# Performance work log

Hardware: AMD Instinct MI355X
Metric: run time of the kernel (lower is better)

## Reference

```python
import jax, jax.numpy as jnp
import numpy as np

D_INNER, D_STATE, DT_RANK, D_CONV, NBLK = 256, 8, 8, 4, 3

def _conv2d(x, w, b=None):
    y = jax.lax.conv_general_dilated(x, w, (1, 1), 'SAME', dimension_numbers=('NCHW', 'OIHW', 'NCHW'))
    return y if b is None else y + b[None, :, None, None]

def _ln(x, g, b, eps=1e-5):
    m = x.mean(-1, keepdims=True)
    v = x.var(-1, keepdims=True)
    return (x - m) / jnp.sqrt(v + eps) * g + b

def _bn(x, g, b, m, v, eps=1e-5):
    return (x - m[None, :, None, None]) / jnp.sqrt(v[None, :, None, None] + eps) * g[None, :, None, None] + b[None, :, None, None]

def _up2(x):
    return jnp.repeat(jnp.repeat(x, 2, axis=2), 2, axis=3)

def _silu(x):
    return x * jax.nn.sigmoid(x)

def _selective_scan(u, dt, A, Bm, Cm):
    # u, dt: (B,L,D); A: (D,N); Bm, Cm: (B,L,N)
    dA = jnp.exp(dt[..., None] * A)              # (B,L,D,N)
    dBu = (dt * u)[..., None] * Bm[:, :, None, :]
    h0 = jnp.zeros((u.shape[0], u.shape[2], A.shape[1]), u.dtype)
    def step(h, inp):
        dA_t, dBu_t, C_t = inp
        h = dA_t * h + dBu_t
        return h, jnp.einsum('bdn,bn->bd', h, C_t)
    _, ys = jax.lax.scan(step, h0, (jnp.moveaxis(dA, 1, 0), jnp.moveaxis(dBu, 1, 0), jnp.moveaxis(Cm, 1, 0)))
    return jnp.moveaxis(ys, 0, 1)                # (B,L,D)

def _mamba(x, in_w, conv_w, conv_b, xproj_w, dt_w, dt_b, Alog, Dp, out_w):
    xz = jnp.einsum('bld,ed->ble', x, in_w)      # (B,L,2*D_INNER)
    xm, z = jnp.split(xz, 2, axis=-1)
    xc = jnp.moveaxis(xm, 1, 2)                  # (B,D,L)
    xc = jax.lax.conv_general_dilated(xc, conv_w[:, None, :], (1,), [(D_CONV - 1, 0)], dimension_numbers=('NCH', 'OIH', 'NCH'), feature_group_count=D_INNER)
    xm = _silu(jnp.moveaxis(xc + conv_b[None, :, None], 2, 1))
    xdbl = jnp.einsum('bld,ed->ble', xm, xproj_w)
    dt, Bm, Cm = jnp.split(xdbl, [DT_RANK, DT_RANK + D_STATE], axis=-1)
    dt = jax.nn.softplus(jnp.einsum('blr,dr->bld', dt, dt_w) + dt_b)
    A = -jnp.exp(Alog)
    y = _selective_scan(xm, dt, A, Bm, Cm) + xm * Dp
    y = y * _silu(z)
    return jnp.einsum('bld,od->blo', y, out_w)

def _cce(inp, ref, w1, w2):
    a = _conv2d(inp, w1)
    r = _conv2d(ref, w2)
    gate = jax.nn.sigmoid(a.max(axis=(2, 3), keepdims=True) + a.mean(axis=(2, 3), keepdims=True))
    return r * gate


def setup_inputs() -> dict:
    key = jax.random.key(0)
    ks = jax.random.split(key, 24)
    s = 0.05
    inp = {}
    inp['fused'] = jax.random.normal(ks[0], (16, 1024, 128), jnp.float32)
    inp['orig_x'] = jax.random.uniform(ks[1], (16, 32, 128, 128), jnp.float32)
    inp['orig_y'] = jax.random.uniform(ks[2], (16, 32, 128, 128), jnp.float32)
    inp['m_ln_g'] = jnp.ones((NBLK, 128), jnp.float32)
    inp['m_ln_b'] = jnp.zeros((NBLK, 128), jnp.float32)
    inp['m_in_w'] = jax.random.normal(ks[3], (NBLK, 2 * D_INNER, 128), jnp.float32) * s
    inp['m_conv_w'] = jax.random.normal(ks[4], (NBLK, D_INNER, D_CONV), jnp.float32) * s
    inp['m_conv_b'] = jnp.zeros((NBLK, D_INNER), jnp.float32)
    inp['m_xproj_w'] = jax.random.normal(ks[5], (NBLK, DT_RANK + 2 * D_STATE, D_INNER), jnp.float32) * s
    inp['m_dt_w'] = jax.random.normal(ks[6], (NBLK, D_INNER, DT_RANK), jnp.float32) * s
    inp['m_dt_b'] = jax.random.normal(ks[7], (NBLK, D_INNER), jnp.float32) * 0.1
    inp['m_Alog'] = jnp.log(jnp.broadcast_to(jnp.arange(1, D_STATE + 1, dtype=jnp.float32), (NBLK, D_INNER, D_STATE)))
    inp['m_D'] = jnp.ones((NBLK, D_INNER), jnp.float32)
    inp['m_out_w'] = jax.random.normal(ks[8], (NBLK, 128, D_INNER), jnp.float32) * s
    inp['lnf_g'] = jnp.ones((128,), jnp.float32)
    inp['lnf_b'] = jnp.zeros((128,), jnp.float32)
    inp['c1_w'] = jax.random.normal(ks[9], (64, 128, 3, 3), jnp.float32) * s
    inp['c1_b'] = jnp.zeros((64,), jnp.float32)
    inp['bn1_g'] = jnp.ones((64,), jnp.float32)
    inp['bn1_b'] = jnp.zeros((64,), jnp.float32)
    inp['bn1_m'] = jnp.zeros((64,), jnp.float32)
    inp['bn1_v'] = jnp.ones((64,), jnp.float32)
    inp['c2_w'] = jax.random.normal(ks[10], (32, 64, 3, 3), jnp.float32) * s
    inp['c2_b'] = jnp.zeros((32,), jnp.float32)
    inp['bn2_g'] = jnp.ones((32,), jnp.float32)
    inp['bn2_b'] = jnp.zeros((32,), jnp.float32)
    inp['bn2_m'] = jnp.zeros((32,), jnp.float32)
    inp['bn2_v'] = jnp.ones((32,), jnp.float32)
    inp['cce_w1'] = jax.random.normal(ks[11], (32, 32, 1, 1), jnp.float32) * s
    inp['cce_w2'] = jax.random.normal(ks[12], (32, 32, 1, 1), jnp.float32) * s
    inp['c3_w'] = jax.random.normal(ks[13], (1, 32, 3, 3), jnp.float32) * s
    inp['c3_b'] = jnp.zeros((1,), jnp.float32)
    return inp


def reference(fused, orig_x, orig_y, m_ln_g, m_ln_b, m_in_w, m_conv_w, m_conv_b, m_xproj_w, m_dt_w, m_dt_b, m_Alog, m_D, m_out_w, lnf_g, lnf_b, c1_w, c1_b, bn1_g, bn1_b, bn1_m, bn1_v, c2_w, c2_b, bn2_g, bn2_b, bn2_m, bn2_v, cce_w1, cce_w2, c3_w, c3_b):
    # 3 pre-LN Mamba blocks with residual connections
    for i in range(NBLK):
        skip = fused
        h = _ln(fused, m_ln_g[i], m_ln_b[i])
        fused = _mamba(h, m_in_w[i], m_conv_w[i], m_conv_b[i], m_xproj_w[i], m_dt_w[i], m_dt_b[i], m_Alog[i], m_D[i], m_out_w[i]) + skip
    fused = _ln(fused, lnf_g, lnf_b)
    B = fused.shape[0]
    fused = jnp.transpose(fused.reshape(B, 32, 32, 128), (0, 3, 1, 2))  # b c h w
    fused = _up2(fused)
    fused = jax.nn.relu(_bn(_conv2d(fused, c1_w, c1_b), bn1_g, bn1_b, bn1_m, bn1_v))
    fused = _up2(fused)
    fused = _bn(jax.nn.relu(_conv2d(fused, c2_w, c2_b)), bn2_g, bn2_b, bn2_m, bn2_v)
    fused = fused + _cce(orig_x, orig_y, cce_w1, cce_w2)
    fused = fused + _cce(orig_y, orig_x, cce_w1, cce_w2)
    return jax.nn.sigmoid(_conv2d(fused, c3_w, c3_b))
```

## Files before the change

kernel.cpp:

```cpp
#include <hip/hip_runtime.h>
#include <hip/hip_bf16.h>

#define BB   16
#define LL   1024
#define DM   128
#define DIN  256
#define NST  8
#define NROWS (BB*LL)
#define NCH  32
#define TCH  32
#define PSZ  1048576

static __device__ __forceinline__ float sigmoidf_(float x){ return 1.f/(1.f+expf(-x)); }
static __device__ __forceinline__ float siluf_(float x){ return x/(1.f+expf(-x)); }
static __device__ __forceinline__ unsigned short f2bf(float f){
    union { float f; unsigned u; } v; v.f = f;
    unsigned r = v.u + 0x7fff + ((v.u >> 16) & 1);
    return (unsigned short)(r >> 16);
}

typedef __attribute__((ext_vector_type(8))) short short8;
typedef __attribute__((ext_vector_type(4))) float floatx4;

__global__ __launch_bounds__(64) void ln_kernel(const float* __restrict__ X,
        const float* __restrict__ g, const float* __restrict__ b,
        float* __restrict__ Y, int transpose)
{
    int row = blockIdx.x;
    int t = threadIdx.x;
    float x0 = X[(long)row*DM + t];
    float x1 = X[(long)row*DM + 64 + t];
    float s = x0 + x1, ss = x0*x0 + x1*x1;
    #pragma unroll
    for (int off = 32; off; off >>= 1) { s += __shfl_down(s, off); ss += __shfl_down(ss, off); }
    s = __shfl(s, 0); ss = __shfl(ss, 0);
    float mean = s * (1.f/128.f);
    float var  = ss * (1.f/128.f) - mean*mean;
    float inv  = rsqrtf(var + 1e-5f);
    float y0 = (x0-mean)*inv*g[t]    + b[t];
    float y1 = (x1-mean)*inv*g[64+t] + b[64+t];
    if (!transpose) {
        Y[(long)row*DM + t] = y0;
        Y[(long)row*DM + 64 + t] = y1;
    } else {
        int bb = row >> 10, l = row & 1023;
        Y[((long)(bb*DM) + t)*LL + l] = y0;
        Y[((long)(bb*DM) + 64 + t)*LL + l] = y1;
    }
}

__global__ __launch_bounds__(64) void ln_bf16_kernel(const float* __restrict__ X,
        const float* __restrict__ g, const float* __restrict__ b,
        unsigned short* __restrict__ Y)
{
    int row = blockIdx.x;
    int t = threadIdx.x;
    float x0 = X[(long)row*DM + t];
    float x1 = X[(long)row*DM + 64 + t];
    float s = x0 + x1, ss = x0*x0 + x1*x1;
    #pragma unroll
    for (int off = 32; off; off >>= 1) { s += __shfl_down(s, off); ss += __shfl_down(ss, off); }
    s = __shfl(s, 0); ss = __shfl(ss, 0);
    float mean = s * (1.f/128.f);
    float var  = ss * (1.f/128.f) - mean*mean;
    float inv  = rsqrtf(var + 1e-5f);
    Y[(long)row*DM + t]      = f2bf((x0-mean)*inv*g[t]    + b[t]);
    Y[(long)row*DM + 64 + t] = f2bf((x1-mean)*inv*g[64+t] + b[64+t]);
}

__global__ void wcvt(const float* __restrict__ Win, const float* __restrict__ Wout,
                     unsigned short* __restrict__ Wb)
{
    int t = blockIdx.x*256 + threadIdx.x;
    if (t < 196608) Wb[t] = f2bf(Win[t]);
    else if (t < 294912) Wb[t] = f2bf(Wout[t - 196608]);
}

template<int K, int MT>
__global__ __launch_bounds__(256) void gemm_bf16(const unsigned short* __restrict__ A,
        const unsigned short* __restrict__ Wb, const float* __restrict__ S,
        float* __restrict__ C, int N)
{
    constexpr int NMT = MT/64;
    __shared__ unsigned short Als[MT][40];
    __shared__ unsigned short Bls[128][40];
    const int tid = threadIdx.x;
    const int m0 = blockIdx.x * MT;
    const int n0 = blockIdx.y * 128;
    const int lane = tid & 63, wv = tid >> 6;
    const int fr = lane & 15, quad = lane >> 4;
    floatx4 acc[NMT][8];
    #pragma unroll
    for (int mt = 0; mt < NMT; mt++)
        #pragma unroll
        for (int nt = 0; nt < 8; nt++) acc[mt][nt] = (floatx4){0.f,0.f,0.f,0.f};
    for (int kc = 0; kc < K; kc += 32) {
        __syncthreads();
        #pragma unroll
        for (int u = tid; u < MT*4; u += 256) {
            int row = u >> 2, seg = u & 3;
            *(uint4*)&Als[row][seg*8] = *(const uint4*)&A[(long)(m0+row)*K + kc + seg*8];
        }
        #pragma unroll
        for (int u = tid; u < 512; u += 256) {
            int row = u >> 2, seg = u & 3;
            *(uint4*)&Bls[row][seg*8] = *(const uint4*)&Wb[(long)(n0+row)*K + kc + seg*8];
        }
        __syncthreads();
        short8 af[NMT];
        #pragma unroll
        for (int mt = 0; mt < NMT; mt++)
            af[mt] = *(const short8*)&Als[wv*(16*NMT) + mt*16 + fr][quad*8];
        #pragma unroll
        for (int nt = 0; nt < 8; nt++) {
            short8 bfv = *(const short8*)&Bls[nt*16 + fr][quad*8];
            #pragma unroll
            for (int mt = 0; mt < NMT; mt++)
                acc[mt][nt] = __builtin_amdgcn_mfma_f32_16x16x32_bf16(af[mt], bfv, acc[mt][nt], 0, 0, 0);
        }
    }
    const int rq = quad * 4;
    #pragma unroll
    for (int mt = 0; mt < NMT; mt++)
        #pragma unroll
        for (int nt = 0; nt < 8; nt++)
            #pragma unroll
            for (int r = 0; r < 4; r++) {
                long m = m0 + wv*(16*NMT) + mt*16 + rq + r;
                long n = n0 + nt*16 + fr;
                float v = acc[mt][nt][r];
                if (S) v += S[m*N + n];
                C[m*N + n] = v;
            }
}

__global__ __launch_bounds__(256) void dwconv_xproj(const float* __restrict__ xz,
        const float* __restrict__ cw, const float* __restrict__ cb,
        const float* __restrict__ xproj_w, const float* __restrict__ dt_w,
        const float* __restrict__ dt_b, float* __restrict__ xc,
        float* __restrict__ dt_out, float* __restrict__ BC)
{
    __shared__ float xs[DIN];
    __shared__ float xdbl[24];
    int bl = blockIdx.x;
    int d  = threadIdx.x;
    int l  = bl & 1023;
    float w0 = cw[d*4+0], w1 = cw[d*4+1], w2 = cw[d*4+2], w3 = cw[d*4+3];
    const float* base = xz + (long)bl*512 + d;
    float acc = cb[d] + w3 * base[0];
    if (l >= 1) acc += w2 * base[-512];
    if (l >= 2) acc += w1 * base[-1024];
    if (l >= 3) acc += w0 * base[-1536];
    float u = siluf_(acc);
    xs[d] = u;
    xc[(long)bl*DIN + d] = u;
    __syncthreads();
    int t = d;
    if (t < 192) {
        int e = t >> 3, j = t & 7;
        float p = 0.f;
        for (int k = j; k < DIN; k += 8) p += xs[k] * xproj_w[e*DIN + k];
        p += __shfl_down(p, 4, 8);
        p += __shfl_down(p, 2, 8);
        p += __shfl_down(p, 1, 8);
        if (j == 0) xdbl[e] = p;
    }
    __syncthreads();
    float v = dt_b[d];
    #pragma unroll
    for (int r = 0; r < 8; r++) v += xdbl[r] * dt_w[d*8 + r];
    v = (v > 20.f) ? v : log1pf(expf(v));
    dt_out[(long)bl*DIN + d] = v;
    if (t < 16) BC[(long)bl*16 + t] = xdbl[8 + t];
}

__global__ __launch_bounds__(256) void scan_part(const float* __restrict__ dt,
        const float* __restrict__ xc, const float* __restrict__ BC,
        const float* __restrict__ Alog, float* __restrict__ PS)
{
    int b = blockIdx.x, c = blockIdx.y;
    int d = threadIdx.x;
    float a[NST], P[NST], S[NST];
    #pragma unroll
    for (int n = 0; n < NST; n++) { a[n] = -expf(Alog[d*NST + n]); P[n] = 1.f; S[n] = 0.f; }
    int t0 = c*TCH;
    const float* dtp = dt + ((long)b*LL + t0)*DIN + d;
    const float* up  = xc + ((long)b*LL + t0)*DIN + d;
    const float* bc  = BC + ((long)b*LL + t0)*16;
    for (int t = 0; t < TCH; t++) {
        float dtv = dtp[(long)t*DIN];
        float u   = up[(long)t*DIN];
        const float4* bc4 = (const float4*)(bc + t*16);
        float4 B0 = bc4[0], B1 = bc4[1];
        float Bv[NST] = {B0.x,B0.y,B0.z,B0.w,B1.x,B1.y,B1.z,B1.w};
        float dtu = dtv * u;
        #pragma unroll
        for (int n = 0; n < NST; n++) {
            float dA = __expf(dtv * a[n]);
            S[n] = dA * S[n] + dtu * Bv[n];
            P[n] *= dA;
        }
    }
    long o = (((long)b*NCH + c)*DIN + d)*8;
    #pragma unroll
    for (int n = 0; n < NST; n++) { PS[o + n] = P[n]; PS[PSZ + o + n] = S[n]; }
}

__global__ __launch_bounds__(256) void scan_mid(const float* __restrict__ PS,
        float* __restrict__ Hinit)
{
    int b = blockIdx.x;
    int n = blockIdx.y;
    int d = threadIdx.x;
    float h = 0.f;
    for (int c = 0; c < NCH; c++) {
        long o = (((long)b*NCH + c)*DIN + d)*8 + n;
        Hinit[o] = h;
        h = PS[o] * h + PS[PSZ + o];
    }
}

__global__ __launch_bounds__(256) void scan_fin(const float* __restrict__ dt,
        const float* __restrict__ xc, const float* __restrict__ BC,
        const float* __restrict__ xz, const float* __restrict__ Alog,
        const float* __restrict__ Dp, const float* __restrict__ Hinit,
        unsigned short* __restrict__ yg)
{
    int b = blockIdx.x, c = blockIdx.y;
    int d = threadIdx.x;
    float a[NST], h[NST];
    long o = (((long)b*NCH + c)*DIN + d)*8;
    #pragma unroll
    for (int n = 0; n < NST; n++) { a[n] = -expf(Alog[d*NST + n]); h[n] = Hinit[o + n]; }
    float Dpd = Dp[d];
    int t0 = c*TCH;
    const float* dtp = dt + ((long)b*LL + t0)*DIN + d;
    const float* up  = xc + ((long)b*LL + t0)*DIN + d;
    const float* bc  = BC + ((long)b*LL + t0)*16;
    const float* zp  = xz + ((long)b*LL + t0)*512 + 256 + d;
    unsigned short* yo = yg + ((long)b*LL + t0)*DIN + d;
    for (int t = 0; t < TCH; t++) {
        float dtv = dtp[(long)t*DIN];
        float u   = up[(long)t*DIN];
        const float4* bc4 = (const float4*)(bc + t*16);
        float4 B0 = bc4[0], B1 = bc4[1], C0 = bc4[2], C1 = bc4[3];
        float Bv[NST] = {B0.x,B0.y,B0.z,B0.w,B1.x,B1.y,B1.z,B1.w};
        float Cv[NST] = {C0.x,C0.y,C0.z,C0.w,C1.x,C1.y,C1.z,C1.w};
        float dtu = dtv * u;
        float y = 0.f;
        #pragma unroll
        for (int n = 0; n < NST; n++) {
            float dA = __expf(dtv * a[n]);
            h[n] = dA * h[n] + dtu * Bv[n];
            y += h[n] * Cv[n];
        }
        y += u * Dpd;
        float z = zp[(long)t*512];
        yo[(long)t*DIN] = f2bf(y * siluf_(z));
    }
}

__global__ void prep_weff(const float* __restrict__ Wr, float* __restrict__ We, int total)
{
    int t = blockIdx.x*256 + threadIdx.x;
    if (t >= total) return;
    float w[3][3];
    #pragma unroll
    for (int a = 0; a < 3; a++)
        #pragma unroll
        for (int c = 0; c < 3; c++) w[a][c] = Wr[(long)t*9 + a*3 + c];
    float cw[2][3][2];
    #pragma unroll
    for (int ky = 0; ky < 3; ky++) {
        cw[0][ky][0] = w[ky][0];           cw[0][ky][1] = w[ky][1] + w[ky][2];
        cw[1][ky][0] = w[ky][0] + w[ky][1]; cw[1][ky][1] = w[ky][2];
    }
    float* o = We + (long)t*16;
    #pragma unroll
    for (int px = 0; px < 2; px++) {
        o[0*8+px*4+0] = cw[px][0][0];               o[0*8+px*4+1] = cw[px][0][1];
        o[0*8+px*4+2] = cw[px][1][0]+cw[px][2][0];  o[0*8+px*4+3] = cw[px][1][1]+cw[px][2][1];
        o[1*8+px*4+0] = cw[px][0][0]+cw[px][1][0];  o[1*8+px*4+1] = cw[px][0][1]+cw[px][1][1];
        o[1*8+px*4+2] = cw[px][2][0];               o[1*8+px*4+3] = cw[px][2][1];
    }
}

template<int CIN, int INW, int ICB>
__global__ __launch_bounds__(256) void conv_up2_phase(const float* __restrict__ X,
        const float* __restrict__ We, const float* __restrict__ bias,
        const float* __restrict__ bng, const float* __restrict__ bnb,
        const float* __restrict__ bnm, const float* __restrict__ bnv,
        float* __restrict__ Y, int relu_first, int COUT)
{
    constexpr int OUTW = 2*INW;
    constexpr int NXT  = OUTW/64;
    __shared__ float  src[ICB][6][34];
    __shared__ float4 wf[ICB][16][4];
    const int ys = blockIdx.x / NXT, xt = blockIdx.x % NXT;
    const int y0 = ys*8, x0 = xt*64;
    const int ocb = blockIdx.y * 16;
    const int b = blockIdx.z;
    const int tid = threadIdx.x;
    const int rel = tid & 63, ocq = tid >> 6;
    const int Xc = x0 + rel;
    const int px = Xc & 1;
    const int lcp = (rel >> 1) + px;
    const int ry0 = y0 >> 1;
    float acc[8][4] = {};
    for (int ic0 = 0; ic0 < CIN; ic0 += ICB) {
        __syncthreads();
        for (int i = tid; i < ICB*6*34; i += 256) {
            int ic = i / 204, rem = i % 204;
            int rr = rem / 34, cc = rem % 34;
            int gr = ry0 - 1 + rr, gc = (x0>>1) - 1 + cc;
            float v = 0.f;
            if ((unsigned)gr < (unsigned)INW && (unsigned)gc < (unsigned)INW)
                v = X[((long)(b*CIN + ic0+ic))*(INW*INW) + gr*INW + gc];
            src[ic][rr][cc] = v;
        }
        for (int i = tid; i < ICB*256; i += 256) {
            int ic = i >> 8, rem = i & 255;
            int ol = rem >> 4, k = rem & 15;
            ((float*)&wf[ic][ol][0])[k] = We[((long)(ocb+ol)*CIN + ic0+ic)*16 + k];
        }
        __syncthreads();
        for (int ic = 0; ic < ICB; ic++) {
            float s[6][2];
            #pragma unroll
            for (int r = 0; r < 6; r++) { s[r][0] = src[ic][r][lcp]; s[r][1] = src[ic][r][lcp+1]; }
            #pragma unroll
            for (int ol = 0; ol < 4; ol++) {
                float4 w0 = wf[ic][(ocq<<2)+ol][px];
                float4 w1 = wf[ic][(ocq<<2)+ol][2+px];
                #pragma unroll
                for (int p = 0; p < 4; p++) {
                    acc[2*p  ][ol] += w0.x*s[p  ][0] + w0.y*s[p  ][1] + w0.z*s[p+1][0] + w0.w*s[p+1][1];
                    acc[2*p+1][ol] += w1.x*s[p+1][0] + w1.y*s[p+1][1] + w1.z*s[p+2][0] + w1.w*s[p+2][1];
                }
            }
        }
    }
    #pragma unroll
    for (int ol = 0; ol < 4; ol++) {
        int oc = ocb + (ocq<<2) + ol;
        float bi = bias[oc];
        float sc = bng[oc] * rsqrtf(bnv[oc] + 1e-5f);
        float sh = bnb[oc] - bnm[oc]*sc;
        #pragma unroll
        for (int yy = 0; yy < 8; yy++) {
            float v = acc[yy][ol] + bi;
            v = relu_first ? (fmaxf(v, 0.f)*sc + sh) : fmaxf(v*sc + sh, 0.f);
            Y[((long)(b*COUT + oc))*(OUTW*OUTW) + (long)(y0+yy)*OUTW + Xc] = v;
        }
    }
}

__global__ __launch_bounds__(256) void cce_gate_partial(const float* __restrict__ ox,
        const float* __restrict__ oy, const float* __restrict__ w1,
        float* __restrict__ pmax, float* __restrict__ psum)
{
    __shared__ float xs[32*512];
    __shared__ float wl[32*32];
    __shared__ float rmx[4][32], rsm[4][32];
    const int sg = blockIdx.x;
    const int dir = blockIdx.y, b = blockIdx.z;
    const float* X = (dir == 0 ? ox : oy) + (long)b*524288;
    const int t = threadIdx.x;
    for (int i = t; i < 1024; i += 256) { int oc = i >> 5, ic = i & 31; wl[ic*32 + oc] = w1[i]; }
    const int ocg = t & 3, pslot = t >> 2;
    const int oc0 = ocg*8;
    float mx[8], sm[8];
    #pragma unroll
    for (int j = 0; j < 8; j++) { mx[j] = -1e30f; sm[j] = 0.f; }
    const int base = sg*1024;
    for (int tile = 0; tile < 2; tile++) {
        __syncthreads();
        const int p0 = base + tile*512;
        for (int i = t*4; i < 32*512; i += 1024) {
            int ic = i >> 9, px = i & 511;
            *(float4*)&xs[ic*512 + px] = *(const float4*)&X[(long)ic*16384 + p0 + px];
        }
        __syncthreads();
        float acc[8][8];
        #pragma unroll
        for (int p = 0; p < 8; p++)
            #pragma unroll
            for (int j = 0; j < 8; j++) acc[p][j] = 0.f;
        #pragma unroll
        for (int ic = 0; ic < 32; ic++) {
            float4 x0 = *(const float4*)&xs[ic*512 + pslot*4];
            float4 x1 = *(const float4*)&xs[ic*512 + 256 + pslot*4];
            float4 wa = *(const float4*)&wl[ic*32 + oc0];
            float4 wb = *(const float4*)&wl[ic*32 + oc0 + 4];
            float xv[8] = {x0.x,x0.y,x0.z,x0.w,x1.x,x1.y,x1.z,x1.w};
            float wv[8] = {wa.x,wa.y,wa.z,wa.w,wb.x,wb.y,wb.z,wb.w};
            #pragma unroll
            for (int p = 0; p < 8; p++)
                #pragma unroll
                for (int j = 0; j < 8; j++)
                    acc[p][j] += xv[p]*wv[j];
        }
        #pragma unroll
        for (int p = 0; p < 8; p++)
            #pragma unroll
            for (int j = 0; j < 8; j++) { mx[j] = fmaxf(mx[j], acc[p][j]); sm[j] += acc[p][j]; }
    }
    #pragma unroll
    for (int j = 0; j < 8; j++) {
        #pragma unroll
        for (int off = 32; off >= 4; off >>= 1) {
            mx[j] = fmaxf(mx[j], __shfl_down(mx[j], off));
            sm[j] += __shfl_down(sm[j], off);
        }
    }
    const int wave = t >> 6, lane = t & 63;
    __syncthreads();
    if (lane < 4) {
        #pragma unroll
        for (int j = 0; j < 8; j++) { rmx[wave][lane*8+j] = mx[j]; rsm[wave][lane*8+j] = sm[j]; }
    }
    __syncthreads();
    if (t < 32) {
        float M = fmaxf(fmaxf(rmx[0][t], rmx[1][t]), fmaxf(rmx[2][t], rmx[3][t]));
        float S = rsm[0][t] + rsm[1][t] + rsm[2][t] + rsm[3][t];
        long idx = ((long)(dir*16 + b)*32 + t)*16 + sg;
        pmax[idx] = M; psum[idx] = S;
    }
}

__global__ void cce_gate_finish(const float* __restrict__ pmax, const float* __restrict__ psum,
                                float* __restrict__ gates)
{
    int i = blockIdx.x*64 + threadIdx.x;
    if (i < 1024) {
        float M = -1e30f, S = 0.f;
        #pragma unroll
        for (int sg = 0; sg < 16; sg++) { M = fmaxf(M, pmax[i*16+sg]); S += psum[i*16+sg]; }
        gates[i] = sigmoidf_(M + S*(1.f/16384.f));
    }
}

__global__ __launch_bounds__(256) void cce_add(const float* __restrict__ ox,
        const float* __restrict__ oy, const float* __restrict__ w2,
        const float* __restrict__ gates, float* __restrict__ v)
{
    __shared__ float w[32][32];
    int t = threadIdx.x;
    int b = blockIdx.y;
    int s = blockIdx.x*256 + t;
    for (int i = t; i < 1024; i += 256) w[i>>5][i&31] = w2[i];
    __syncthreads();
    const float* xb = ox + (long)b*524288;
    const float* yb = oy + (long)b*524288;
    float r1[32] = {}, r2[32] = {};
    for (int ic = 0; ic < 32; ic++) {
        float xv = xb[(long)ic*16384 + s];
        float yv = yb[(long)ic*16384 + s];
        #pragma unroll
        for (int oc = 0; oc < 32; oc++) { r1[oc] += w[oc][ic]*yv; r2[oc] += w[oc][ic]*xv; }
    }
    float* vb = v + (long)b*524288;
    const float* g1 = gates + b*32;
    const float* g2 = gates + 512 + b*32;
    #pragma unroll
    for (int oc = 0; oc < 32; oc++)
        vb[(long)oc*16384 + s] += g1[oc]*r1[oc] + g2[oc]*r2[oc];
}

__global__ __launch_bounds__(256) void conv3_sig(const float* __restrict__ v,
        const float* __restrict__ w3, const float* __restrict__ b3, float* __restrict__ out)
{
    __shared__ float w[288];
    int t = threadIdx.x;
    for (int i = t; i < 288; i += 256) w[i] = w3[i];
    __syncthreads();
    int b = blockIdx.y;
    int y = blockIdx.x*2 + (t >> 7);
    int x = t & 127;
    const float* vb = v + (long)b*524288;
    float acc = b3[0];
    for (int ic = 0; ic < 32; ic++) {
        const float* p = vb + (long)ic*16384;
        #pragma unroll
        for (int ky = 0; ky < 3; ky++) {
            int yy = y + ky - 1;
            if ((unsigned)yy >= 128u) continue;
            #pragma unroll
            for (int kx = 0; kx < 3; kx++) {
                int xx = x + kx - 1;
                if ((unsigned)xx >= 128u) continue;
                acc += w[ic*9 + ky*3 + kx] * p[yy*128 + xx];
            }
        }
    }
    out[(long)b*16384 + y*128 + x] = sigmoidf_(acc);
}

extern "C" void kernel_launch(void* const* d_in, const int* in_sizes, int n_in,
                              void* d_out, int out_size, void* d_ws, size_t ws_size,
                              hipStream_t stream)
{
    const float* fused_in = (const float*)d_in[0];
    const float* orig_x   = (const float*)d_in[1];
    const float* orig_y   = (const float*)d_in[2];
    const float* m_ln_g   = (const float*)d_in[3];
    const float* m_ln_b   = (const float*)d_in[4];
    const float* m_in_w   = (const float*)d_in[5];
    const float* m_conv_w = (const float*)d_in[6];
    const float* m_conv_b = (const float*)d_in[7];
    const float* m_xproj_w= (const float*)d_in[8];
    const float* m_dt_w   = (const float*)d_in[9];
    const float* m_dt_b   = (const float*)d_in[10];
    const float* m_Alog   = (const float*)d_in[11];
    const float* m_D      = (const float*)d_in[12];
    const float* m_out_w  = (const float*)d_in[13];
    const float* lnf_g    = (const float*)d_in[14];
    const float* lnf_b    = (const float*)d_in[15];
    const float* c1_w     = (const float*)d_in[16];
    const float* c1_b     = (const float*)d_in[17];
    const float* bn1_g    = (const float*)d_in[18];
    const float* bn1_b    = (const float*)d_in[19];
    const float* bn1_m    = (const float*)d_in[20];
    const float* bn1_v    = (const float*)d_in[21];
    const float* c2_w     = (const float*)d_in[22];
    const float* c2_b     = (const float*)d_in[23];
    const float* bn2_g    = (const float*)d_in[24];
    const float* bn2_b    = (const float*)d_in[25];
    const float* bn2_m    = (const float*)d_in[26];
    const float* bn2_v    = (const float*)d_in[27];
    const float* cce_w1   = (const float*)d_in[28];
    const float* cce_w2   = (const float*)d_in[29];
    const float* c3_w     = (const float*)d_in[30];
    const float* c3_b     = (const float*)d_in[31];

    float* W = (float*)d_ws;
    float* fusedA = W;
    float* fusedB = W + 2097152;
    float* xzb    = W + 4194304;
    float* xcb    = W + 12582912;
    float* dtb    = W + 16777216;
    float* ygb    = W + 20971520;
    float* BCb    = W + 25165824;
    float* gates  = W + 25427968;
    float* Hinit  = W + 25445376;
    float* pmax   = W + 26493952;
    float* psum   = W + 26510336;
    unsigned short* xlnb = (unsigned short*)ygb;
    unsigned short* ygbb = (unsigned short*)ygb;
    unsigned short* wbf  = ((unsigned short*)ygb) + 4194304;
    float* tb  = xzb;
    float* c1b = xcb;
    float* vb  = dtb;
    float* weff1 = BCb;
    float* weff2 = BCb + 131072;

    cce_gate_partial<<<dim3(16,2,16), 256, 0, stream>>>(orig_x, orig_y, cce_w1, pmax, psum);
    cce_gate_finish<<<16, 64, 0, stream>>>(pmax, psum, gates);

    wcvt<<<1152, 256, 0, stream>>>(m_in_w, m_out_w, wbf);

    const float* cur = fused_in;
    float* nxt = fusedA;
    for (int i = 0; i < 3; i++) {
        ln_bf16_kernel<<<NROWS, 64, 0, stream>>>(cur, m_ln_g + i*128, m_ln_b + i*128, xlnb);
        gemm_bf16<128,128><<<dim3(128, 4), 256, 0, stream>>>(xlnb, wbf + (long)i*65536, nullptr, xzb, 512);
        dwconv_xproj<<<NROWS, 256, 0, stream>>>(xzb, m_conv_w + i*1024, m_conv_b + i*256,
                m_xproj_w + i*24*256, m_dt_w + i*2048, m_dt_b + i*256, xcb, dtb, BCb);
        scan_part<<<dim3(BB, NCH), 256, 0, stream>>>(dtb, xcb, BCb, m_Alog + i*2048, nxt);
        scan_mid<<<dim3(BB, NST), 256, 0, stream>>>(nxt, Hinit);
        scan_fin<<<dim3(BB, NCH), 256, 0, stream>>>(dtb, xcb, BCb, xzb, m_Alog + i*2048, m_D + i*256, Hinit, ygbb);
        gemm_bf16<256,64><<<dim3(256, 1), 256, 0, stream>>>(ygbb, wbf + 196608 + (long)i*32768, cur, nxt, 128);
        cur = nxt;
        nxt = (i == 0) ? fusedB : fusedA;
    }
    ln_kernel<<<NROWS, 64, 0, stream>>>(cur, lnf_g, lnf_b, tb, 1);
    prep_weff<<<32, 256, 0, stream>>>(c1_w, weff1, 64*128);
    prep_weff<<<8, 256, 0, stream>>>(c2_w, weff2, 32*64);
    conv_up2_phase<128, 32, 16><<<dim3(8, 4, 16), 256, 0, stream>>>(tb, weff1, c1_b, bn1_g, bn1_b, bn1_m, bn1_v, c1b, 0, 64);
    conv_up2_phase<64, 64, 16><<<dim3(32, 2, 16), 256, 0, stream>>>(c1b, weff2, c2_b, bn2_g, bn2_b, bn2_m, bn2_v, vb, 1, 32);
    cce_add<<<dim3(64, 16), 256, 0, stream>>>(orig_x, orig_y, cce_w2, gates, vb);
    conv3_sig<<<dim3(64, 16), 256, 0, stream>>>(vb, c3_w, c3_b, (float*)d_out);
}
```

Baseline: 893.9 us.

## Restructure upsample-conv kernels to read wave-uniform weights from global memory

The phase-decomposed upsample+conv kernels now assign each wavefront a fixed column phase and row pair, so the weight index is wave-uniform (made explicit with readfirstlane) and weights are read straight from global memory as scalar/broadcast loads instead of being staged through shared memory. The weight prep kernel rewrites the effective weights in a [phase][cin][cout][8] layout to match, and each thread now holds 16 output channels by 2 rows instead of 4 channels by 8 rows. This removes the LDS weight staging and its reads, but each thread reuses fewer input values across rows and does more weight loads per FMA.

```diff
diff --git a/kernel.cpp b/kernel.cpp
--- a/kernel.cpp
+++ b/kernel.cpp
@@ -260,10 +260,12 @@
     }
 }
 
-__global__ void prep_weff(const float* __restrict__ Wr, float* __restrict__ We, int total)
+__global__ void prep_weff2(const float* __restrict__ Wr, float* __restrict__ We,
+                           int CIN, int COUT)
 {
     int t = blockIdx.x*256 + threadIdx.x;
-    if (t >= total) return;
+    if (t >= CIN*COUT) return;
+    int oc = t / CIN, ic = t % CIN;
     float w[3][3];
     #pragma unroll
     for (int a = 0; a < 3; a++)
@@ -272,21 +274,21 @@
     float cw[2][3][2];
     #pragma unroll
     for (int ky = 0; ky < 3; ky++) {
-        cw[0][ky][0] = w[ky][0];           cw[0][ky][1] = w[ky][1] + w[ky][2];
+        cw[0][ky][0] = w[ky][0];            cw[0][ky][1] = w[ky][1] + w[ky][2];
         cw[1][ky][0] = w[ky][0] + w[ky][1]; cw[1][ky][1] = w[ky][2];
     }
-    float* o = We + (long)t*16;
     #pragma unroll
     for (int px = 0; px < 2; px++) {
-        o[0*8+px*4+0] = cw[px][0][0];               o[0*8+px*4+1] = cw[px][0][1];
-        o[0*8+px*4+2] = cw[px][1][0]+cw[px][2][0];  o[0*8+px*4+3] = cw[px][1][1]+cw[px][2][1];
-        o[1*8+px*4+0] = cw[px][0][0]+cw[px][1][0];  o[1*8+px*4+1] = cw[px][0][1]+cw[px][1][1];
-        o[1*8+px*4+2] = cw[px][2][0];               o[1*8+px*4+3] = cw[px][2][1];
+        float* o = We + ((long)(px*CIN + ic)*COUT + oc)*8;
+        o[0] = cw[px][0][0];               o[1] = cw[px][0][1];
+        o[2] = cw[px][1][0]+cw[px][2][0];  o[3] = cw[px][1][1]+cw[px][2][1];
+        o[4] = cw[px][0][0]+cw[px][1][0];  o[5] = cw[px][0][1]+cw[px][1][1];
+        o[6] = cw[px][2][0];               o[7] = cw[px][2][1];
     }
 }
 
 template<int CIN, int INW, int ICB>
-__global__ __launch_bounds__(256) void conv_up2_phase(const float* __restrict__ X,
+__global__ __launch_bounds__(256) void conv_up2_sm(const float* __restrict__ X,
         const float* __restrict__ We, const float* __restrict__ bias,
         const float* __restrict__ bng, const float* __restrict__ bnb,
         const float* __restrict__ bnm, const float* __restrict__ bnv,
@@ -294,64 +296,60 @@
 {
     constexpr int OUTW = 2*INW;
     constexpr int NXT  = OUTW/64;
-    __shared__ float  src[ICB][6][34];
-    __shared__ float4 wf[ICB][16][4];
+    __shared__ float src[ICB][6][34];
     const int ys = blockIdx.x / NXT, xt = blockIdx.x % NXT;
     const int y0 = ys*8, x0 = xt*64;
     const int ocb = blockIdx.y * 16;
     const int b = blockIdx.z;
     const int tid = threadIdx.x;
-    const int rel = tid & 63, ocq = tid >> 6;
-    const int Xc = x0 + rel;
-    const int px = Xc & 1;
-    const int lcp = (rel >> 1) + px;
+    const int wvu = __builtin_amdgcn_readfirstlane(tid >> 6);
+    const int px = wvu & 1, g = wvu >> 1;
+    const int lane = tid & 63;
+    const int r = lane >> 5, hc = lane & 31;
+    const int p = g*2 + r;
+    const int cc = hc + px;
     const int ry0 = y0 >> 1;
-    float acc[8][4] = {};
+    float acc[16][2] = {};
     for (int ic0 = 0; ic0 < CIN; ic0 += ICB) {
         __syncthreads();
         for (int i = tid; i < ICB*6*34; i += 256) {
             int ic = i / 204, rem = i % 204;
-            int rr = rem / 34, cc = rem % 34;
-            int gr = ry0 - 1 + rr, gc = (x0>>1) - 1 + cc;
+            int rr = rem / 34, ccs = rem % 34;
+            int gr = ry0 - 1 + rr, gc = (x0>>1) - 1 + ccs;
             float v = 0.f;
             if ((unsigned)gr < (unsigned)INW && (unsigned)gc < (unsigned)INW)
                 v = X[((long)(b*CIN + ic0+ic))*(INW*INW) + gr*INW + gc];
-            src[ic][rr][cc] = v;
-        }
-        for (int i = tid; i < ICB*256; i += 256) {
-            int ic = i >> 8, rem = i & 255;
-            int ol = rem >> 4, k = rem & 15;
-            ((float*)&wf[ic][ol][0])[k] = We[((long)(ocb+ol)*CIN + ic0+ic)*16 + k];
+            src[ic][rr][ccs] = v;
         }
         __syncthreads();
         for (int ic = 0; ic < ICB; ic++) {
-            float s[6][2];
-            #pragma unroll
-            for (int r = 0; r < 6; r++) { s[r][0] = src[ic][r][lcp]; s[r][1] = src[ic][r][lcp+1]; }
-            #pragma unroll
-            for (int ol = 0; ol < 4; ol++) {
-                float4 w0 = wf[ic][(ocq<<2)+ol][px];
-                float4 w1 = wf[ic][(ocq<<2)+ol][2+px];
-                #pragma unroll
-                for (int p = 0; p < 4; p++) {
-                    acc[2*p  ][ol] += w0.x*s[p  ][0] + w0.y*s[p  ][1] + w0.z*s[p+1][0] + w0.w*s[p+1][1];
-                    acc[2*p+1][ol] += w1.x*s[p+1][0] + w1.y*s[p+1][1] + w1.z*s[p+2][0] + w1.w*s[p+2][1];
-                }
+            float s00 = src[ic][p  ][cc], s01 = src[ic][p  ][cc+1];
+            float s10 = src[ic][p+1][cc], s11 = src[ic][p+1][cc+1];
+            float s20 = src[ic][p+2][cc], s21 = src[ic][p+2][cc+1];
+            const float* wb = We + ((long)(px*CIN + ic0+ic)*COUT + ocb)*8;
+            #pragma unroll
+            for (int oc = 0; oc < 16; oc++) {
+                float4 w0 = *(const float4*)&wb[oc*8];
+                float4 w1 = *(const float4*)&wb[oc*8 + 4];
+                acc[oc][0] += w0.x*s00 + w0.y*s01 + w0.z*s10 + w0.w*s11;
+                acc[oc][1] += w1.x*s10 + w1.y*s11 + w1.z*s20 + w1.w*s21;
             }
         }
     }
-    #pragma unroll
-    for (int ol = 0; ol < 4; ol++) {
-        int oc = ocb + (ocq<<2) + ol;
-        float bi = bias[oc];
-        float sc = bng[oc] * rsqrtf(bnv[oc] + 1e-5f);
-        float sh = bnb[oc] - bnm[oc]*sc;
-        #pragma unroll
-        for (int yy = 0; yy < 8; yy++) {
-            float v = acc[yy][ol] + bi;
-            v = relu_first ? (fmaxf(v, 0.f)*sc + sh) : fmaxf(v*sc + sh, 0.f);
-            Y[((long)(b*COUT + oc))*(OUTW*OUTW) + (long)(y0+yy)*OUTW + Xc] = v;
-        }
+    const int Xc = x0 + 2*hc + px;
+    #pragma unroll
+    for (int oc = 0; oc < 16; oc++) {
+        int o = ocb + oc;
+        float bi = bias[o];
+        float sc = bng[o] * rsqrtf(bnv[o] + 1e-5f);
+        float sh = bnb[o] - bnm[o]*sc;
+        float v0 = acc[oc][0] + bi;
+        float v1 = acc[oc][1] + bi;
+        v0 = relu_first ? (fmaxf(v0, 0.f)*sc + sh) : fmaxf(v0*sc + sh, 0.f);
+        v1 = relu_first ? (fmaxf(v1, 0.f)*sc + sh) : fmaxf(v1*sc + sh, 0.f);
+        long base = ((long)(b*COUT + o))*(OUTW*OUTW) + (long)(y0 + 2*p)*OUTW + Xc;
+        Y[base]        = v0;
+        Y[base + OUTW] = v1;
     }
 }
 
@@ -574,10 +572,10 @@
         nxt = (i == 0) ? fusedB : fusedA;
     }
     ln_kernel<<<NROWS, 64, 0, stream>>>(cur, lnf_g, lnf_b, tb, 1);
-    prep_weff<<<32, 256, 0, stream>>>(c1_w, weff1, 64*128);
-    prep_weff<<<8, 256, 0, stream>>>(c2_w, weff2, 32*64);
-    conv_up2_phase<128, 32, 16><<<dim3(8, 4, 16), 256, 0, stream>>>(tb, weff1, c1_b, bn1_g, bn1_b, bn1_m, bn1_v, c1b, 0, 64);
-    conv_up2_phase<64, 64, 16><<<dim3(32, 2, 16), 256, 0, stream>>>(c1b, weff2, c2_b, bn2_g, bn2_b, bn2_m, bn2_v, vb, 1, 32);
+    prep_weff2<<<32, 256, 0, stream>>>(c1_w, weff1, 128, 64);
+    prep_weff2<<<8, 256, 0, stream>>>(c2_w, weff2, 64, 32);
+    conv_up2_sm<128, 32, 16><<<dim3(8, 4, 16), 256, 0, stream>>>(tb, weff1, c1_b, bn1_g, bn1_b, bn1_m, bn1_v, c1b, 0, 64);
+    conv_up2_sm<64, 64, 16><<<dim3(32, 2, 16), 256, 0, stream>>>(c1b, weff2, c2_b, bn2_g, bn2_b, bn2_m, bn2_v, vb, 1, 32);
     cce_add<<<dim3(64, 16), 256, 0, stream>>>(orig_x, orig_y, cce_w2, gates, vb);
     conv3_sig<<<dim3(64, 16), 256, 0, stream>>>(vb, c3_w, c3_b, (float*)d_out);
 }
```

New measurement: 966.4 us. 8.1% more time.

## Use zero-padded activation buffers and read conv inputs directly without shared staging

Applied to the files above, without the earlier changes.

The final LayerNorm and the first upsample-conv now write into spatially zero-padded buffers, with border zeroing done by a new small kernel. This lets the upsample convolutions drop their shared-memory tiling, barriers and bounds checks. Each thread reads its input rows and folded weights straight from global memory through the caches. The cost is redundant global and cache traffic, since threads no longer share staged tiles, plus two extra small launches.

```diff
diff --git a/kernel.cpp b/kernel.cpp
--- a/kernel.cpp
+++ b/kernel.cpp
@@ -44,8 +44,9 @@
         Y[(long)row*DM + 64 + t] = y1;
     } else {
         int bb = row >> 10, l = row & 1023;
-        Y[((long)(bb*DM) + t)*LL + l] = y0;
-        Y[((long)(bb*DM) + 64 + t)*LL + l] = y1;
+        int r = l >> 5, c = l & 31;
+        Y[((long)(bb*DM + t)*34 + (r+1))*34 + (c+1)]      = y0;
+        Y[((long)(bb*DM + 64 + t)*34 + (r+1))*34 + (c+1)] = y1;
     }
 }
 
@@ -260,6 +261,19 @@
     }
 }
 
+__global__ void zpad(float* __restrict__ buf, int NP, int P)
+{
+    int t = blockIdx.x*256 + threadIdx.x;
+    int per = 4*P - 4;
+    if (t >= NP*per) return;
+    int pl = t / per, k = t % per;
+    int r, c;
+    if (k < P)        { r = 0;     c = k; }
+    else if (k < 2*P) { r = P-1;   c = k - P; }
+    else { int kk = k - 2*P; r = 1 + (kk >> 1); c = (kk & 1) ? (P-1) : 0; }
+    buf[(long)pl*P*P + (long)r*P + c] = 0.f;
+}
+
 __global__ void prep_weff(const float* __restrict__ Wr, float* __restrict__ We, int total)
 {
     int t = blockIdx.x*256 + threadIdx.x;
@@ -285,8 +299,8 @@
     }
 }
 
-template<int CIN, int INW, int ICB>
-__global__ __launch_bounds__(256) void conv_up2_phase(const float* __restrict__ X,
+template<int CIN, int INW, int OPAD>
+__global__ __launch_bounds__(256) void conv_up2_reg(const float* __restrict__ X,
         const float* __restrict__ We, const float* __restrict__ bias,
         const float* __restrict__ bng, const float* __restrict__ bnb,
         const float* __restrict__ bnm, const float* __restrict__ bnv,
@@ -294,8 +308,8 @@
 {
     constexpr int OUTW = 2*INW;
     constexpr int NXT  = OUTW/64;
-    __shared__ float  src[ICB][6][34];
-    __shared__ float4 wf[ICB][16][4];
+    constexpr int PW   = INW + 2;
+    constexpr int OW   = OUTW + 2*OPAD;
     const int ys = blockIdx.x / NXT, xt = blockIdx.x % NXT;
     const int y0 = ys*8, x0 = xt*64;
     const int ocb = blockIdx.y * 16;
@@ -307,38 +321,28 @@
     const int lcp = (rel >> 1) + px;
     const int ry0 = y0 >> 1;
     float acc[8][4] = {};
-    for (int ic0 = 0; ic0 < CIN; ic0 += ICB) {
-        __syncthreads();
-        for (int i = tid; i < ICB*6*34; i += 256) {
-            int ic = i / 204, rem = i % 204;
-            int rr = rem / 34, cc = rem % 34;
-            int gr = ry0 - 1 + rr, gc = (x0>>1) - 1 + cc;
-            float v = 0.f;
-            if ((unsigned)gr < (unsigned)INW && (unsigned)gc < (unsigned)INW)
-                v = X[((long)(b*CIN + ic0+ic))*(INW*INW) + gr*INW + gc];
-            src[ic][rr][cc] = v;
-        }
-        for (int i = tid; i < ICB*256; i += 256) {
-            int ic = i >> 8, rem = i & 255;
-            int ol = rem >> 4, k = rem & 15;
-            ((float*)&wf[ic][ol][0])[k] = We[((long)(ocb+ol)*CIN + ic0+ic)*16 + k];
-        }
-        __syncthreads();
-        for (int ic = 0; ic < ICB; ic++) {
-            float s[6][2];
-            #pragma unroll
-            for (int r = 0; r < 6; r++) { s[r][0] = src[ic][r][lcp]; s[r][1] = src[ic][r][lcp+1]; }
-            #pragma unroll
-            for (int ol = 0; ol < 4; ol++) {
-                float4 w0 = wf[ic][(ocq<<2)+ol][px];
-                float4 w1 = wf[ic][(ocq<<2)+ol][2+px];
-                #pragma unroll
-                for (int p = 0; p < 4; p++) {
-                    acc[2*p  ][ol] += w0.x*s[p  ][0] + w0.y*s[p  ][1] + w0.z*s[p+1][0] + w0.w*s[p+1][1];
-                    acc[2*p+1][ol] += w1.x*s[p+1][0] + w1.y*s[p+1][1] + w1.z*s[p+2][0] + w1.w*s[p+2][1];
-                }
+    const float* sp = X + (long)(b*CIN)*(PW*PW) + (long)ry0*PW + (x0>>1) + lcp;
+    const float* wp0 = We + ((long)(ocb + (ocq<<2))*CIN)*16 + px*4;
+    const float* wp1 = wp0 + (long)CIN*16;
+    const float* wp2 = wp1 + (long)CIN*16;
+    const float* wp3 = wp2 + (long)CIN*16;
+    for (int ic = 0; ic < CIN; ic++) {
+        float s[6][2];
+        #pragma unroll
+        for (int r = 0; r < 6; r++) { s[r][0] = sp[r*PW]; s[r][1] = sp[r*PW + 1]; }
+        const float* wps[4] = {wp0, wp1, wp2, wp3};
+        #pragma unroll
+        for (int ol = 0; ol < 4; ol++) {
+            float4 w0 = *(const float4*)wps[ol];
+            float4 w1 = *(const float4*)(wps[ol] + 8);
+            #pragma unroll
+            for (int p = 0; p < 4; p++) {
+                acc[2*p  ][ol] += w0.x*s[p  ][0] + w0.y*s[p  ][1] + w0.z*s[p+1][0] + w0.w*s[p+1][1];
+                acc[2*p+1][ol] += w1.x*s[p+1][0] + w1.y*s[p+1][1] + w1.z*s[p+2][0] + w1.w*s[p+2][1];
             }
         }
+        sp  += PW*PW;
+        wp0 += 16; wp1 += 16; wp2 += 16; wp3 += 16;
     }
     #pragma unroll
     for (int ol = 0; ol < 4; ol++) {
@@ -350,7 +354,7 @@
         for (int yy = 0; yy < 8; yy++) {
             float v = acc[yy][ol] + bi;
             v = relu_first ? (fmaxf(v, 0.f)*sc + sh) : fmaxf(v*sc + sh, 0.f);
-            Y[((long)(b*COUT + oc))*(OUTW*OUTW) + (long)(y0+yy)*OUTW + Xc] = v;
+            Y[((long)(b*COUT + oc))*(OW*OW) + (long)(y0+yy+OPAD)*OW + (Xc+OPAD)] = v;
         }
     }
 }
@@ -548,8 +552,8 @@
     unsigned short* xlnb = (unsigned short*)ygb;
     unsigned short* ygbb = (unsigned short*)ygb;
     unsigned short* wbf  = ((unsigned short*)ygb) + 4194304;
-    float* tb  = xzb;
-    float* c1b = xcb;
+    float* tb_pad  = xzb;
+    float* c1b_pad = xzb + 2367488;
     float* vb  = dtb;
     float* weff1 = BCb;
     float* weff2 = BCb + 131072;
@@ -573,11 +577,13 @@
         cur = nxt;
         nxt = (i == 0) ? fusedB : fusedA;
     }
-    ln_kernel<<<NROWS, 64, 0, stream>>>(cur, lnf_g, lnf_b, tb, 1);
+    zpad<<<1056, 256, 0, stream>>>(tb_pad, 2048, 34);
+    zpad<<<1040, 256, 0, stream>>>(c1b_pad, 1024, 66);
+    ln_kernel<<<NROWS, 64, 0, stream>>>(cur, lnf_g, lnf_b, tb_pad, 1);
     prep_weff<<<32, 256, 0, stream>>>(c1_w, weff1, 64*128);
     prep_weff<<<8, 256, 0, stream>>>(c2_w, weff2, 32*64);
-    conv_up2_phase<128, 32, 16><<<dim3(8, 4, 16), 256, 0, stream>>>(tb, weff1, c1_b, bn1_g, bn1_b, bn1_m, bn1_v, c1b, 0, 64);
-    conv_up2_phase<64, 64, 16><<<dim3(32, 2, 16), 256, 0, stream>>>(c1b, weff2, c2_b, bn2_g, bn2_b, bn2_m, bn2_v, vb, 1, 32);
+    conv_up2_reg<128, 32, 1><<<dim3(8, 4, 16), 256, 0, stream>>>(tb_pad, weff1, c1_b, bn1_g, bn1_b, bn1_m, bn1_v, c1b_pad, 0, 64);
+    conv_up2_reg<64, 64, 0><<<dim3(32, 2, 16), 256, 0, stream>>>(c1b_pad, weff2, c2_b, bn2_g, bn2_b, bn2_m, bn2_v, vb, 1, 32);
     cce_add<<<dim3(64, 16), 256, 0, stream>>>(orig_x, orig_y, cce_w2, gates, vb);
     conv3_sig<<<dim3(64, 16), 256, 0, stream>>>(vb, c3_w, c3_b, (float*)d_out);
 }
```

Result: slower. 934.3 us (+4.5%).
